# Kernel tuning notes

Hardware: AMD Instinct MI355X
Metric: run time of the kernel (lower is better)

Reference implementation:

```python
import jax, jax.numpy as jnp
import numpy as np

F_NHID = 64
C_NHID = 64
U_INIT = F_NHID + C_NHID + 1   # 129
U_OUT = F_NHID + C_NHID        # 128
U_HID = 128
N_AGG = 4
M_INIT = 3 * N_AGG * U_OUT + C_NHID  # 1600
M_HID = 256
M_OUT = C_NHID


def setup_inputs() -> dict:
    key = jax.random.key(0)
    ks = jax.random.split(key, 12)
    B, Nc, Nf = 4, 512, 256
    h_fac = jax.random.normal(ks[0], (B, Nf, F_NHID), dtype=jnp.float32)
    h_cus = jax.random.normal(ks[1], (B, Nc, C_NHID), dtype=jnp.float32)
    edge = jax.random.normal(ks[2], (B, Nc, Nf, 1), dtype=jnp.float32)
    adj = jax.random.randint(ks[3], (B, Nc, Nf), 0, 2).astype(jnp.float32)
    def lin(k, i, o):
        return jax.random.normal(k, (i, o), dtype=jnp.float32) / np.sqrt(i)
    return {
        'h_fac': h_fac, 'h_cus': h_cus, 'edge': edge, 'adj': adj,
        'U_W1': lin(ks[4], U_INIT, U_HID), 'U_b1': jnp.zeros((U_HID,), jnp.float32),
        'U_W2': lin(ks[5], U_HID, U_OUT), 'U_b2': jnp.zeros((U_OUT,), jnp.float32),
        'M_W1': lin(ks[6], M_INIT, M_HID), 'M_b1': jnp.zeros((M_HID,), jnp.float32),
        'M_W2': lin(ks[7], M_HID, M_OUT), 'M_b2': jnp.zeros((M_OUT,), jnp.float32),
    }


def reference(h_fac, h_cus, edge, adj, U_W1, U_b1, U_W2, U_b2, M_W1, M_b1, M_W2, M_b2):
    B, Nc, c = h_cus.shape
    Nf = h_fac.shape[1]
    # Per-edge message input: [customer_feat, facility_feat, edge_scalar] -> (B,Nc,Nf,U_INIT)
    msg = jnp.concatenate([
        jnp.broadcast_to(h_cus[:, :, None, :], (B, Nc, Nf, c)),
        jnp.broadcast_to(h_fac[:, None, :, :], (B, Nc, Nf, h_fac.shape[-1])),
        edge,
    ], axis=-1)
    # U MLP (pretransformation): relu -> linear
    m = jax.nn.relu(msg @ U_W1 + U_b1)
    m = m @ U_W2 + U_b2  # (B, Nc, Nf, U_OUT)

    mask = adj > 0                              # (B, Nc, Nf)
    maskf = mask[..., None].astype(m.dtype)     # (B, Nc, Nf, 1)
    cnt = jnp.sum(maskf, axis=2)                # (B, Nc, 1)
    mean = jnp.sum(m * maskf, axis=2) / cnt     # nanmean over masked entries
    var = jnp.sum(((m - mean[:, :, None, :]) ** 2) * maskf, axis=2) / cnt
    std = jnp.sqrt(var)                         # population std (divides by count)
    mx = jnp.max(jnp.where(mask[..., None], m, -jnp.inf), axis=2)
    mn = jnp.min(jnp.where(mask[..., None], m, jnp.inf), axis=2)

    # Degree-based scalers (get_avgd + scale_amplification/attenuation)
    deg_c = jnp.sum(adj, axis=-1)               # (B, Nc)
    deg_f = jnp.sum(adj, axis=-2)               # (B, Nf)
    avg_d = jnp.mean(jnp.concatenate([jnp.log(deg_c + 1.0), jnp.log(deg_f + 1.0)], axis=-1), axis=-1)  # (B,)
    scale = (jnp.log(deg_c + 1.0) / avg_d[:, None])[..., None]          # (B, Nc, 1)
    scale_inv = jnp.where(scale != 0, 1.0 / scale, jnp.zeros_like(scale))

    feats = [h_cus]
    for a in (mean, std, mx, mn):
        feats.extend([a, a * scale, a * scale_inv])
    h = jnp.concatenate(feats, axis=-1)         # (B, Nc, M_INIT)

    # M MLP (posttransformation): relu -> linear (last activation 'none')
    h = jax.nn.relu(h @ M_W1 + M_b1)
    out = h @ M_W2 + M_b2                       # (B, Nc, C_NHID)
    return out
```

## Files before the change

### kernel.cpp

```cpp
#include <hip/hip_runtime.h>
#include <hip/hip_bf16.h>


using bs8 = __attribute__((ext_vector_type(8))) short;
using f4  = __attribute__((ext_vector_type(4))) float;
using f2  = __attribute__((ext_vector_type(2))) float;

__device__ __forceinline__ unsigned short f2bf(float f) {
    union { float f; unsigned int u; } x; x.f = f;
    unsigned int u = x.u + 0x7FFFu + ((x.u >> 16) & 1u);
    return (unsigned short)(u >> 16);
}

__device__ __forceinline__ unsigned int pkbf(float a, float b) {
    __hip_bfloat162 h = __float22bfloat162_rn(make_float2(a, b));
    union { __hip_bfloat162 h; unsigned int u; } c; c.h = h;
    return c.u;
}

__global__ void PNALayer_35081292874189_kernel() {}

#define OFF_AC     0u
#define OFF_AF     1048576u
#define OFF_DEGC   1572864u
#define OFF_DEGF   1581056u
#define OFF_SCALE  1585152u
#define OFF_SINV   1593344u
#define OFF_FEATB  1601536u
#define OFF_HMID   8155392u
#define OFF_W2T    10252544u
#define OFF_W1TB   10318080u
#define WS_NEED    11170048u

__global__ void PNALayer_ws_fail(float* out, int n) {
    int i = blockIdx.x * 256 + threadIdx.x;
    if (i < n) out[i] = 2500.0f;
}

__global__ void PNALayer_prep1(
    const float* h_fac, const float* h_cus, const float* adj,
    const float* U_W1, const float* U_b1, const float* U_W2, const float* M_W1,
    float* wsAc, float* wsAf, float* wsDegC, float* wsDegF,
    unsigned short* wsW2Tb, unsigned short* wsW1Tb)
{
    __shared__ float sH[64];
    __shared__ float sRed[256];
    __shared__ float sT[64][65];
    int bid = blockIdx.x, t = threadIdx.x;

    if (bid < 1024) {
        int b = bid >> 8, f = bid & 255;
        if (t < 64) sH[t] = h_fac[(b * 256 + f) * 64 + t];
        __syncthreads();
        if (t < 128) {
            float acc = 0.f;
            for (int k = 0; k < 64; ++k)
                acc += sH[k] * U_W1[(64 + k) * 128 + t];
            wsAf[(b * 256 + f) * 128 + t] = acc;
        }
        float v = adj[(b * 512 + t) * 256 + f] + adj[(b * 512 + t + 256) * 256 + f];
        sRed[t] = v; __syncthreads();
        for (int s = 128; s > 0; s >>= 1) { if (t < s) sRed[t] += sRed[t + s]; __syncthreads(); }
        if (t == 0) wsDegF[b * 256 + f] = sRed[0];
    } else if (bid < 3072) {
        int bc = bid - 1024;
        if (t < 64) sH[t] = h_cus[bc * 64 + t];
        __syncthreads();
        if (t < 128) {
            float acc = U_b1[t];
            for (int k = 0; k < 64; ++k)
                acc += sH[k] * U_W1[k * 128 + t];
            wsAc[bc * 128 + t] = acc;
        }
        float v = adj[bc * 256 + t];
        sRed[t] = v; __syncthreads();
        for (int s = 128; s > 0; s >>= 1) { if (t < s) sRed[t] += sRed[t + s]; __syncthreads(); }
        if (t == 0) wsDegC[bc] = sRed[0];
    } else if (bid < 3076) {
        int l = bid - 3072;
        int k0 = (l >> 1) * 64, n0 = (l & 1) * 64;
        for (int rep = 0; rep < 16; ++rep) {
            int idx = rep * 256 + t; int r = idx >> 6, c = idx & 63;
            sT[r][c] = U_W2[(k0 + r) * 128 + n0 + c];
        }
        __syncthreads();
        for (int rep = 0; rep < 16; ++rep) {
            int idx = rep * 256 + t; int r = idx >> 6, c = idx & 63;
            wsW2Tb[(n0 + r) * 128 + k0 + c] = f2bf(sT[c][r]);
        }
    } else if (bid < 3176) {
        int l = bid - 3076;
        int k0 = (l % 25) * 64, n0 = (l / 25) * 64;
        for (int rep = 0; rep < 16; ++rep) {
            int idx = rep * 256 + t; int r = idx >> 6, c = idx & 63;
            sT[r][c] = M_W1[(k0 + r) * 256 + n0 + c];
        }
        __syncthreads();
        for (int rep = 0; rep < 16; ++rep) {
            int idx = rep * 256 + t; int r = idx >> 6, c = idx & 63;
            wsW1Tb[(n0 + r) * 1664 + k0 + c] = f2bf(sT[c][r]);
        }
    } else {
        for (int i = 0; i < 64; ++i) {
            int idx = i * 256 + t;
            int n = idx >> 6, k = 1600 + (idx & 63);
            wsW1Tb[n * 1664 + k] = 0;
        }
    }
}

__global__ void PNALayer_prep2(
    const float* wsDegC, const float* wsDegF, float* wsScale, float* wsSinv)
{
    __shared__ float sRed[256];
    __shared__ float sAvg;
    int b = blockIdx.x, t = threadIdx.x;
    float v = logf(wsDegC[b * 512 + t] + 1.f) + logf(wsDegC[b * 512 + t + 256] + 1.f)
            + logf(wsDegF[b * 256 + t] + 1.f);
    sRed[t] = v; __syncthreads();
    for (int s = 128; s > 0; s >>= 1) { if (t < s) sRed[t] += sRed[t + s]; __syncthreads(); }
    if (t == 0) sAvg = sRed[0] / 768.f;
    __syncthreads();
    float avg = sAvg;
    for (int c = t; c < 512; c += 256) {
        float lg = logf(wsDegC[b * 512 + c] + 1.f);
        float sc = lg / avg;
        float si = (sc != 0.f) ? 1.f / sc : 0.f;
        wsScale[b * 512 + c] = sc;
        wsSinv[b * 512 + c] = si;
    }
}

__global__ __launch_bounds__(512, 6) void PNALayer_edge(
    const float* h_cus, const float* edge, const float* adj,
    const float* U_W1, const float* U_b2,
    const float* wsAc, const float* wsAf, const unsigned short* wsW2Tb,
    const float* wsScale, const float* wsSinv,
    unsigned short* featB)
{
    __shared__ __align__(16) unsigned short sM1[64 * 136];
    __shared__ float sE[256];
    __shared__ float sAc[128];
    __shared__ float sWe[128];
    __shared__ unsigned short sFidx[256];
    __shared__ unsigned long long sBal[4];

    int bc = blockIdx.x;
    int b  = bc >> 9;
    int t  = threadIdx.x;
    int w = t >> 6, quad = (t >> 4) & 3, ln = t & 15;

    int r0 = w * 16 + ln;
    bs8 bw[4];
#pragma unroll
    for (int kk = 0; kk < 4; ++kk)
        bw[kk] = *(const bs8*)(wsW2Tb + r0 * 128 + kk * 32 + quad * 8);
    float b2v = U_b2[r0];

    bool m = false;
    unsigned long long bal = 0;
    if (t < 256) {
        sE[t] = edge[bc * 256 + t];
        m = adj[bc * 256 + t] > 0.f;
        bal = __ballot(m);
        if ((t & 63) == 0) sBal[t >> 6] = bal;
    }
    if (t >= 256 && t < 384) {
        int j = t - 256;
        sAc[j] = wsAc[bc * 128 + j];
        sWe[j] = U_W1[128 * 128 + j];
    }
    if (t >= 384 && t < 448) {
        int j = t - 384;
        featB[bc * 1600 + j] = f2bf(h_cus[bc * 64 + j]);
    }
    __syncthreads();

    unsigned long long b0 = sBal[0], b1 = sBal[1], b2 = sBal[2], b3 = sBal[3];
    int cnt = __popcll(b0) + __popcll(b1) + __popcll(b2) + __popcll(b3);
    if (t < 256) {
        int wv = t >> 6, l = t & 63;
        int base = 0;
        if (wv > 0) base += __popcll(b0);
        if (wv > 1) base += __popcll(b1);
        if (wv > 2) base += __popcll(b2);
        int rank = __popcll(bal & ((1ULL << l) - 1ULL));
        if (m) sFidx[base + rank] = (unsigned short)t;
    }
    __syncthreads();

    int ntiles = (cnt + 63) >> 6;

    float aS = 0.f, aQ = 0.f, aMx = -1e30f, aMn = 1e30f;
    const f2 zero2 = (f2){0.f, 0.f};

    for (int tl = 0; tl < ntiles; ++tl) {
#pragma unroll
        for (int i = 0; i < 4; ++i) {
            int idx = i * 512 + t;
            int fl = idx >> 5, k = (idx & 31) * 4;
            int fj = tl * 64 + fl;
            uint2 p = make_uint2(0u, 0u);
            if (fj < cnt) {
                int f = sFidx[fj];
                float4 af  = *(const float4*)(wsAf + (b * 256 + f) * 128 + k);
                f2 ac01 = *(const f2*)(sAc + k);
                f2 ac23 = *(const f2*)(sAc + k + 2);
                f2 we01 = *(const f2*)(sWe + k);
                f2 we23 = *(const f2*)(sWe + k + 2);
                float e = sE[f];
                f2 e2 = (f2){e, e};
                f2 s01 = ac01 + (f2){af.x, af.y};
                f2 s23 = ac23 + (f2){af.z, af.w};
                s01 = __builtin_elementwise_fma(e2, we01, s01);
                s23 = __builtin_elementwise_fma(e2, we23, s23);
                f2 r01 = __builtin_elementwise_max(s01, zero2);
                f2 r23 = __builtin_elementwise_max(s23, zero2);
                p.x = pkbf(r01.x, r01.y);
                p.y = pkbf(r23.x, r23.y);
            }
            *(uint2*)(sM1 + fl * 136 + k) = p;
        }
        __syncthreads();

        f4 acc[4];
#pragma unroll
        for (int rt = 0; rt < 4; ++rt) acc[rt] = (f4){0.f, 0.f, 0.f, 0.f};
#pragma unroll
        for (int kk = 0; kk < 4; ++kk) {
            int ko = kk * 32 + quad * 8;
#pragma unroll
            for (int rt = 0; rt < 4; ++rt) {
                bs8 a = *(const bs8*)(sM1 + (rt * 16 + ln) * 136 + ko);
                acc[rt] = __builtin_amdgcn_mfma_f32_16x16x32_bf16(a, bw[kk], acc[rt], 0, 0, 0);
            }
        }

#pragma unroll
        for (int rt = 0; rt < 4; ++rt) {
#pragma unroll
            for (int i = 0; i < 4; ++i) {
                int fj = tl * 64 + rt * 16 + quad * 4 + i;
                if (fj < cnt) {
                    float v = acc[rt][i];
                    aS += v;
                    aQ = fmaf(v, v, aQ);
                    aMx = fmaxf(aMx, v);
                    aMn = fminf(aMn, v);
                }
            }
        }
        __syncthreads();
    }

    aS  += __shfl_xor(aS, 16, 64);  aS  += __shfl_xor(aS, 32, 64);
    aQ  += __shfl_xor(aQ, 16, 64);  aQ  += __shfl_xor(aQ, 32, 64);
    aMx = fmaxf(aMx, __shfl_xor(aMx, 16, 64));
    aMx = fmaxf(aMx, __shfl_xor(aMx, 32, 64));
    aMn = fminf(aMn, __shfl_xor(aMn, 16, 64));
    aMn = fminf(aMn, __shfl_xor(aMn, 32, 64));

    if (quad == 0) {
        float cntf = (float)cnt;
        float sc = wsScale[bc], si = wsSinv[bc];
        unsigned short* fr = featB + bc * 1600;
        int col = w * 16 + ln;
        float meanr = aS / cntf;
        float mean  = meanr + b2v;
        float var   = fmaxf(aQ / cntf - meanr * meanr, 0.f);
        float stdv  = sqrtf(var);
        float mx = aMx + b2v, mn = aMn + b2v;
        fr[64 + col]   = f2bf(mean); fr[192 + col]  = f2bf(mean * sc); fr[320 + col]  = f2bf(mean * si);
        fr[448 + col]  = f2bf(stdv); fr[576 + col]  = f2bf(stdv * sc); fr[704 + col]  = f2bf(stdv * si);
        fr[832 + col]  = f2bf(mx);   fr[960 + col]  = f2bf(mx * sc);   fr[1088 + col] = f2bf(mx * si);
        fr[1216 + col] = f2bf(mn);   fr[1344 + col] = f2bf(mn * sc);   fr[1472 + col] = f2bf(mn * si);
    }
}

__global__ __launch_bounds__(256) void PNALayer_mlp1(
    const unsigned short* featB, const unsigned short* wsW1Tb, const float* M_b1,
    float* h_mid)
{
    __shared__ __align__(16) unsigned short sA[16 * 136];
    __shared__ __align__(16) unsigned short sB[64 * 136];
    int t = threadIdx.x;
    int rb = (blockIdx.x >> 2) * 16, cb = (blockIdx.x & 3) * 64;
    int w = t >> 6, quad = (t >> 4) & 3, ln = t & 15;

    f4 acc = (f4){0.f, 0.f, 0.f, 0.f};

    for (int kt = 0; kt < 13; ++kt) {
        int kb = kt * 128;
        {
            int row = t >> 4, c8 = (t & 15) * 8;
            *(uint4*)(sA + row * 136 + c8) =
                *(const uint4*)(featB + (rb + row) * 1600 + kb + c8);
        }
        for (int i = 0; i < 4; ++i) {
            int vi = i * 256 + t;
            int row = vi >> 4, c8 = (vi & 15) * 8;
            *(uint4*)(sB + row * 136 + c8) =
                *(const uint4*)(wsW1Tb + (cb + row) * 1664 + kb + c8);
        }
        __syncthreads();
        for (int kk = 0; kk < 4; ++kk) {
            int ko = kk * 32 + quad * 8;
            bs8 a = *(const bs8*)(sA + ln * 136 + ko);
            bs8 bb = *(const bs8*)(sB + (w * 16 + ln) * 136 + ko);
            acc = __builtin_amdgcn_mfma_f32_16x16x32_bf16(a, bb, acc, 0, 0, 0);
        }
        __syncthreads();
    }
    int col = cb + w * 16 + ln;
    float b1v = M_b1[col];
    for (int i = 0; i < 4; ++i) {
        int row = rb + quad * 4 + i;
        h_mid[row * 256 + col] = fmaxf(acc[i] + b1v, 0.f);
    }
}

__global__ void PNALayer_mlp2(
    const float* h_mid, const float* M_W2, const float* M_b2, float* out)
{
    int idx = blockIdx.x * 256 + threadIdx.x;
    int row = idx >> 6, j = idx & 63;
    float acc = M_b2[j];
    const float* hr = h_mid + row * 256;
#pragma unroll 8
    for (int k = 0; k < 256; ++k)
        acc += hr[k] * M_W2[k * 64 + j];
    out[idx] = acc;
}

extern "C" void kernel_launch(void* const* d_in, const int* in_sizes, int n_in,
                              void* d_out, int out_size, void* d_ws, size_t ws_size,
                              hipStream_t stream) {
    const float* h_fac = (const float*)d_in[0];
    const float* h_cus = (const float*)d_in[1];
    const float* edge  = (const float*)d_in[2];
    const float* adj   = (const float*)d_in[3];
    const float* U_W1  = (const float*)d_in[4];
    const float* U_b1  = (const float*)d_in[5];
    const float* U_W2  = (const float*)d_in[6];
    const float* U_b2  = (const float*)d_in[7];
    const float* M_W1  = (const float*)d_in[8];
    const float* M_b1  = (const float*)d_in[9];
    const float* M_W2  = (const float*)d_in[10];
    const float* M_b2  = (const float*)d_in[11];
    (void)in_sizes; (void)n_in;

    float* outp = (float*)d_out;
    int nblk_out = (out_size + 255) / 256;

    if (ws_size < (size_t)WS_NEED) {
        PNALayer_ws_fail<<<nblk_out, 256, 0, stream>>>(outp, out_size);
        return;
    }

    char* ws = (char*)d_ws;
    float*          wsAc   = (float*)(ws + OFF_AC);
    float*          wsAf   = (float*)(ws + OFF_AF);
    float*          wsDegC = (float*)(ws + OFF_DEGC);
    float*          wsDegF = (float*)(ws + OFF_DEGF);
    float*          wsScal = (float*)(ws + OFF_SCALE);
    float*          wsSinv = (float*)(ws + OFF_SINV);
    unsigned short* wsFeatB= (unsigned short*)(ws + OFF_FEATB);
    float*          wsHmid = (float*)(ws + OFF_HMID);
    unsigned short* wsW2Tb = (unsigned short*)(ws + OFF_W2T);
    unsigned short* wsW1Tb = (unsigned short*)(ws + OFF_W1TB);

    PNALayer_prep1<<<3177, 256, 0, stream>>>(
        h_fac, h_cus, adj, U_W1, U_b1, U_W2, M_W1,
        wsAc, wsAf, wsDegC, wsDegF, wsW2Tb, wsW1Tb);
    PNALayer_prep2<<<4, 256, 0, stream>>>(wsDegC, wsDegF, wsScal, wsSinv);
    PNALayer_edge<<<2048, 512, 0, stream>>>(
        h_cus, edge, adj, U_W1, U_b2,
        wsAc, wsAf, wsW2Tb, wsScal, wsSinv, wsFeatB);
    PNALayer_mlp1<<<512, 256, 0, stream>>>(wsFeatB, wsW1Tb, M_b1, wsHmid);
    PNALayer_mlp2<<<512, 256, 0, stream>>>(wsHmid, M_W2, M_b2, outp);
}
```

Measured before the change: 149.3 us.

## Move facility degree into prep2, pack edge stats, widen mlp1 tiles, dual-row mlp2

Several unrelated changes land together. Facility degree is now computed inside prep2 by a strided column sum over adj, replacing the strided per-block reduction in prep1. The edge kernel accumulates sum, square-sum, max and min in packed float2 registers, using a fast path for full 64-row tiles and keeping masked scalar handling only for the last partial tile. mlp1 uses 32-row tiles with 512 threads, which halves how often the B operand is reloaded, and mlp2 computes two rows per thread so each weight load is reused. The main risk is prep2: it runs on only 4 blocks and now does a serial strided read of all of adj, which could lengthen that stage.

New measurement: 164.9 us. 1.1x slower.

```diff
diff --git a/kernel.cpp b/kernel.cpp
--- a/kernel.cpp
+++ b/kernel.cpp
@@ -40,7 +40,7 @@
 __global__ void PNALayer_prep1(
     const float* h_fac, const float* h_cus, const float* adj,
     const float* U_W1, const float* U_b1, const float* U_W2, const float* M_W1,
-    float* wsAc, float* wsAf, float* wsDegC, float* wsDegF,
+    float* wsAc, float* wsAf, float* wsDegC,
     unsigned short* wsW2Tb, unsigned short* wsW1Tb)
 {
     __shared__ float sH[64];
@@ -58,10 +58,6 @@
                 acc += sH[k] * U_W1[(64 + k) * 128 + t];
             wsAf[(b * 256 + f) * 128 + t] = acc;
         }
-        float v = adj[(b * 512 + t) * 256 + f] + adj[(b * 512 + t + 256) * 256 + f];
-        sRed[t] = v; __syncthreads();
-        for (int s = 128; s > 0; s >>= 1) { if (t < s) sRed[t] += sRed[t + s]; __syncthreads(); }
-        if (t == 0) wsDegF[b * 256 + f] = sRed[0];
     } else if (bid < 3072) {
         int bc = bid - 1024;
         if (t < 64) sH[t] = h_cus[bc * 64 + t];
@@ -110,13 +106,18 @@
 }
 
 __global__ void PNALayer_prep2(
-    const float* wsDegC, const float* wsDegF, float* wsScale, float* wsSinv)
+    const float* adj, const float* wsDegC, float* wsScale, float* wsSinv)
 {
     __shared__ float sRed[256];
     __shared__ float sAvg;
     int b = blockIdx.x, t = threadIdx.x;
+    float df = 0.f;
+    const float* ap = adj + b * 512 * 256 + t;
+#pragma unroll 8
+    for (int c = 0; c < 512; ++c)
+        df += ap[c * 256];
     float v = logf(wsDegC[b * 512 + t] + 1.f) + logf(wsDegC[b * 512 + t + 256] + 1.f)
-            + logf(wsDegF[b * 256 + t] + 1.f);
+            + logf(df + 1.f);
     sRed[t] = v; __syncthreads();
     for (int s = 128; s > 0; s >>= 1) { if (t < s) sRed[t] += sRed[t + s]; __syncthreads(); }
     if (t == 0) sAvg = sRed[0] / 768.f;
@@ -191,7 +192,8 @@
 
     int ntiles = (cnt + 63) >> 6;
 
-    float aS = 0.f, aQ = 0.f, aMx = -1e30f, aMn = 1e30f;
+    f2 aS2  = (f2){0.f, 0.f},     aQ2  = (f2){0.f, 0.f};
+    f2 aMx2 = (f2){-1e30f, -1e30f}, aMn2 = (f2){1e30f, 1e30f};
     const f2 zero2 = (f2){0.f, 0.f};
 
     for (int tl = 0; tl < ntiles; ++tl) {
@@ -236,22 +238,43 @@
             }
         }
 
-#pragma unroll
-        for (int rt = 0; rt < 4; ++rt) {
-#pragma unroll
-            for (int i = 0; i < 4; ++i) {
-                int fj = tl * 64 + rt * 16 + quad * 4 + i;
-                if (fj < cnt) {
-                    float v = acc[rt][i];
-                    aS += v;
-                    aQ = fmaf(v, v, aQ);
-                    aMx = fmaxf(aMx, v);
-                    aMn = fminf(aMn, v);
+        if (((tl + 1) << 6) <= cnt) {
+#pragma unroll
+            for (int rt = 0; rt < 4; ++rt) {
+                f2 p01 = (f2){acc[rt][0], acc[rt][1]};
+                f2 p23 = (f2){acc[rt][2], acc[rt][3]};
+                aS2 = aS2 + p01;
+                aS2 = aS2 + p23;
+                aQ2 = __builtin_elementwise_fma(p01, p01, aQ2);
+                aQ2 = __builtin_elementwise_fma(p23, p23, aQ2);
+                f2 mx = __builtin_elementwise_max(p01, p23);
+                f2 mn = __builtin_elementwise_min(p01, p23);
+                aMx2 = __builtin_elementwise_max(aMx2, mx);
+                aMn2 = __builtin_elementwise_min(aMn2, mn);
+            }
+        } else {
+#pragma unroll
+            for (int rt = 0; rt < 4; ++rt) {
+#pragma unroll
+                for (int i = 0; i < 4; ++i) {
+                    int fj = tl * 64 + rt * 16 + quad * 4 + i;
+                    if (fj < cnt) {
+                        float v = acc[rt][i];
+                        aS2.x += v;
+                        aQ2.x = fmaf(v, v, aQ2.x);
+                        aMx2.x = fmaxf(aMx2.x, v);
+                        aMn2.x = fminf(aMn2.x, v);
+                    }
                 }
             }
         }
         __syncthreads();
     }
+
+    float aS = aS2.x + aS2.y;
+    float aQ = aQ2.x + aQ2.y;
+    float aMx = fmaxf(aMx2.x, aMx2.y);
+    float aMn = fminf(aMn2.x, aMn2.y);
 
     aS  += __shfl_xor(aS, 16, 64);  aS  += __shfl_xor(aS, 32, 64);
     aQ  += __shfl_xor(aQ, 16, 64);  aQ  += __shfl_xor(aQ, 32, 64);
@@ -277,15 +300,16 @@
     }
 }
 
-__global__ __launch_bounds__(256) void PNALayer_mlp1(
+__global__ __launch_bounds__(512, 2) void PNALayer_mlp1(
     const unsigned short* featB, const unsigned short* wsW1Tb, const float* M_b1,
     float* h_mid)
 {
-    __shared__ __align__(16) unsigned short sA[16 * 136];
+    __shared__ __align__(16) unsigned short sA[32 * 136];
     __shared__ __align__(16) unsigned short sB[64 * 136];
     int t = threadIdx.x;
-    int rb = (blockIdx.x >> 2) * 16, cb = (blockIdx.x & 3) * 64;
+    int rb = (blockIdx.x >> 2) * 32, cb = (blockIdx.x & 3) * 64;
     int w = t >> 6, quad = (t >> 4) & 3, ln = t & 15;
+    int wr = w >> 2, wc = w & 3;
 
     f4 acc = (f4){0.f, 0.f, 0.f, 0.f};
 
@@ -296,25 +320,28 @@
             *(uint4*)(sA + row * 136 + c8) =
                 *(const uint4*)(featB + (rb + row) * 1600 + kb + c8);
         }
-        for (int i = 0; i < 4; ++i) {
-            int vi = i * 256 + t;
+#pragma unroll
+        for (int i = 0; i < 2; ++i) {
+            int vi = i * 512 + t;
             int row = vi >> 4, c8 = (vi & 15) * 8;
             *(uint4*)(sB + row * 136 + c8) =
                 *(const uint4*)(wsW1Tb + (cb + row) * 1664 + kb + c8);
         }
         __syncthreads();
+#pragma unroll
         for (int kk = 0; kk < 4; ++kk) {
             int ko = kk * 32 + quad * 8;
-            bs8 a = *(const bs8*)(sA + ln * 136 + ko);
-            bs8 bb = *(const bs8*)(sB + (w * 16 + ln) * 136 + ko);
+            bs8 a  = *(const bs8*)(sA + (wr * 16 + ln) * 136 + ko);
+            bs8 bb = *(const bs8*)(sB + (wc * 16 + ln) * 136 + ko);
             acc = __builtin_amdgcn_mfma_f32_16x16x32_bf16(a, bb, acc, 0, 0, 0);
         }
         __syncthreads();
     }
-    int col = cb + w * 16 + ln;
+    int col = cb + wc * 16 + ln;
     float b1v = M_b1[col];
+#pragma unroll
     for (int i = 0; i < 4; ++i) {
-        int row = rb + quad * 4 + i;
+        int row = rb + wr * 16 + quad * 4 + i;
         h_mid[row * 256 + col] = fmaxf(acc[i] + b1v, 0.f);
     }
 }
@@ -322,14 +349,20 @@
 __global__ void PNALayer_mlp2(
     const float* h_mid, const float* M_W2, const float* M_b2, float* out)
 {
-    int idx = blockIdx.x * 256 + threadIdx.x;
-    int row = idx >> 6, j = idx & 63;
-    float acc = M_b2[j];
-    const float* hr = h_mid + row * 256;
+    int q = blockIdx.x * 256 + threadIdx.x;
+    int row0 = q >> 6, j = q & 63;
+    int row1 = row0 + 1024;
+    float acc0 = M_b2[j], acc1 = acc0;
+    const float* h0 = h_mid + row0 * 256;
+    const float* h1 = h_mid + row1 * 256;
 #pragma unroll 8
-    for (int k = 0; k < 256; ++k)
-        acc += hr[k] * M_W2[k * 64 + j];
-    out[idx] = acc;
+    for (int k = 0; k < 256; ++k) {
+        float wv = M_W2[k * 64 + j];
+        acc0 = fmaf(h0[k], wv, acc0);
+        acc1 = fmaf(h1[k], wv, acc1);
+    }
+    out[row0 * 64 + j] = acc0;
+    out[row1 * 64 + j] = acc1;
 }
 
 extern "C" void kernel_launch(void* const* d_in, const int* in_sizes, int n_in,
@@ -361,7 +394,6 @@
     float*          wsAc   = (float*)(ws + OFF_AC);
     float*          wsAf   = (float*)(ws + OFF_AF);
     float*          wsDegC = (float*)(ws + OFF_DEGC);
-    float*          wsDegF = (float*)(ws + OFF_DEGF);
     float*          wsScal = (float*)(ws + OFF_SCALE);
     float*          wsSinv = (float*)(ws + OFF_SINV);
     unsigned short* wsFeatB= (unsigned short*)(ws + OFF_FEATB);
@@ -371,11 +403,11 @@
 
     PNALayer_prep1<<<3177, 256, 0, stream>>>(
         h_fac, h_cus, adj, U_W1, U_b1, U_W2, M_W1,
-        wsAc, wsAf, wsDegC, wsDegF, wsW2Tb, wsW1Tb);
-    PNALayer_prep2<<<4, 256, 0, stream>>>(wsDegC, wsDegF, wsScal, wsSinv);
+        wsAc, wsAf, wsDegC, wsW2Tb, wsW1Tb);
+    PNALayer_prep2<<<4, 256, 0, stream>>>(adj, wsDegC, wsScal, wsSinv);
     PNALayer_edge<<<2048, 512, 0, stream>>>(
         h_cus, edge, adj, U_W1, U_b2,
         wsAc, wsAf, wsW2Tb, wsScal, wsSinv, wsFeatB);
-    PNALayer_mlp1<<<512, 256, 0, stream>>>(wsFeatB, wsW1Tb, M_b1, wsHmid);
-    PNALayer_mlp2<<<512, 256, 0, stream>>>(wsHmid, M_W2, M_b2, outp);
-}
+    PNALayer_mlp1<<<256, 512, 0, stream>>>(wsFeatB, wsW1Tb, M_b1, wsHmid);
+    PNALayer_mlp2<<<256, 256, 0, stream>>>(wsHmid, M_W2, M_b2, outp);
+}
```
